# Optimization experiments

Measured on AMD Instinct MI355X. Metric: run time of the kernel, lower is better.

Reference implementation:

```python
import jax, jax.numpy as jnp
import numpy as np

N0, N1, N2 = 80000, 40000, 20000
E1, E2 = 500000, 250000
FIN = 128        # in_channels
H = 2            # heads
C1 = 64          # hidden_channels -> layer1 out per head (concat -> 128)
C2 = 64          # out_channels -> layer2 out per head (mean over heads)
ED = 10          # edge_dim per embedding, total edge feat = 2*ED = 20
NTYPE, NTS = 23, 1158


def setup_inputs() -> dict:
    key = jax.random.key(0)
    ks = jax.random.split(key, 48)
    sc = 0.05
    inp = {
        "x": jax.random.normal(ks[0], (N0, FIN), jnp.float32),
        "ei1_src": jax.random.randint(ks[1], (E1,), 0, N0),
        "ei1_dst": jax.random.randint(ks[2], (E1,), 0, N1),
        "et1": jax.random.randint(ks[3], (E1,), 0, NTYPE),
        "ets1": jax.random.randint(ks[4], (E1,), 0, NTS),
        "ei2_src": jax.random.randint(ks[5], (E2,), 0, N1),
        "ei2_dst": jax.random.randint(ks[6], (E2,), 0, N2),
        "et2": jax.random.randint(ks[7], (E2,), 0, NTYPE),
        "ets2": jax.random.randint(ks[8], (E2,), 0, NTS),
        # shared edge embeddings (Linear(23,10), Linear(1158,10))
        "edge_W": jax.random.normal(ks[9], (ED, NTYPE), jnp.float32) * sc,
        "edge_b": jax.random.normal(ks[10], (ED,), jnp.float32) * sc,
        "time_W": jax.random.normal(ks[11], (ED, NTS), jnp.float32) * sc,
        "time_b": jax.random.normal(ks[12], (ED,), jnp.float32) * sc,
    }
    # layer 1: in=128, heads=2, C=64, concat=True (out dim 128)
    hc1 = H * C1
    inp["Wq1"] = jax.random.normal(ks[13], (hc1, FIN), jnp.float32) * sc
    inp["bq1"] = jnp.zeros((hc1,), jnp.float32)
    inp["Wk1"] = jax.random.normal(ks[14], (hc1, FIN), jnp.float32) * sc
    inp["bk1"] = jnp.zeros((hc1,), jnp.float32)
    inp["Wv1"] = jax.random.normal(ks[15], (hc1, FIN), jnp.float32) * sc
    inp["bv1"] = jnp.zeros((hc1,), jnp.float32)
    inp["We1"] = jax.random.normal(ks[16], (hc1, 2 * ED), jnp.float32) * sc
    inp["Wskip1"] = jax.random.normal(ks[17], (hc1, FIN), jnp.float32) * sc
    inp["bskip1"] = jnp.zeros((hc1,), jnp.float32)
    inp["Wbeta1"] = jax.random.normal(ks[18], (1, 3 * hc1), jnp.float32) * sc
    inp["ln_g"] = jnp.ones((hc1,), jnp.float32)
    inp["ln_b"] = jnp.zeros((hc1,), jnp.float32)
    # layer 2: in=128, heads=2, C=64, concat=False (out dim 64)
    hc2 = H * C2
    inp["Wq2"] = jax.random.normal(ks[19], (hc2, hc1), jnp.float32) * sc
    inp["bq2"] = jnp.zeros((hc2,), jnp.float32)
    inp["Wk2"] = jax.random.normal(ks[20], (hc2, hc1), jnp.float32) * sc
    inp["bk2"] = jnp.zeros((hc2,), jnp.float32)
    inp["Wv2"] = jax.random.normal(ks[21], (hc2, hc1), jnp.float32) * sc
    inp["bv2"] = jnp.zeros((hc2,), jnp.float32)
    inp["We2"] = jax.random.normal(ks[22], (hc2, 2 * ED), jnp.float32) * sc
    inp["Wskip2"] = jax.random.normal(ks[23], (C2, hc1), jnp.float32) * sc
    inp["bskip2"] = jnp.zeros((C2,), jnp.float32)
    inp["Wbeta2"] = jax.random.normal(ks[24], (1, 3 * C2), jnp.float32) * sc
    return inp


def _edge_feat(et, ets, edge_W, edge_b, time_W, time_b):
    # one_hot(e) @ W.T + b == W.T[e] + b (avoids materializing huge one-hot)
    return jnp.concatenate([jnp.take(edge_W.T, et, axis=0) + edge_b,
                            jnp.take(time_W.T, ets, axis=0) + time_b], axis=-1)


def _conv(x_src, x_dst, src, dst, ef, Wq, bq, Wk, bk, Wv, bv, We,
          Wskip, bskip, Wbeta, concat):
    n_dst = x_dst.shape[0]
    HC = Wq.shape[0]
    C = HC // H
    q = (x_dst @ Wq.T + bq).reshape(n_dst, H, C)            # [Nd,H,C]
    k = (x_src @ Wk.T + bk)[src].reshape(-1, H, C)          # [E,H,C]
    v = (x_src @ Wv.T + bv)[src].reshape(-1, H, C)
    e = (ef @ We.T).reshape(-1, H, C)
    k = k + e
    alpha = jnp.einsum('ehc,ehc->eh', q[dst], k) / np.sqrt(C).astype(np.float32)
    # segment softmax over destination nodes
    m = jax.ops.segment_max(alpha, dst, num_segments=n_dst)
    ex = jnp.exp(alpha - m[dst])
    s = jax.ops.segment_sum(ex, dst, num_segments=n_dst)
    a = ex / (s[dst] + 1e-16)                               # [E,H]
    msg = (v + e) * a[..., None]                            # [E,H,C]
    out = jax.ops.segment_sum(msg.reshape(-1, HC), dst, num_segments=n_dst)
    out = out if concat else out.reshape(n_dst, H, C).mean(axis=1)
    x_r = x_dst @ Wskip.T + bskip
    beta = jax.nn.sigmoid(
        jnp.concatenate([out, x_r, out - x_r], axis=-1) @ Wbeta.T)  # [Nd,1]
    return beta * x_r + (1.0 - beta) * out


def _layernorm(x, g, b):
    mu = x.mean(-1, keepdims=True)
    var = x.var(-1, keepdims=True)
    return (x - mu) / jnp.sqrt(var + 1e-5) * g + b


def reference(x, ei1_src, ei1_dst, et1, ets1, ei2_src, ei2_dst, et2, ets2,
              edge_W, edge_b, time_W, time_b,
              Wq1, bq1, Wk1, bk1, Wv1, bv1, We1, Wskip1, bskip1, Wbeta1,
              ln_g, ln_b,
              Wq2, bq2, Wk2, bk2, Wv2, bv2, We2, Wskip2, bskip2, Wbeta2):
    ef1 = _edge_feat(et1, ets1, edge_W, edge_b, time_W, time_b)
    h = _conv(x, x[:N1], ei1_src, ei1_dst, ef1,
              Wq1, bq1, Wk1, bk1, Wv1, bv1, We1, Wskip1, bskip1, Wbeta1,
              concat=True)
    h = jax.nn.gelu(_layernorm(h, ln_g, ln_b), approximate=False)
    ef2 = _edge_feat(et2, ets2, edge_W, edge_b, time_W, time_b)
    o = _conv(h, h[:N2], ei2_src, ei2_dst, ef2,
              Wq2, bq2, Wk2, bk2, Wv2, bv2, We2, Wskip2, bskip2, Wbeta2,
              concat=False)
    return jax.nn.log_softmax(o, axis=-1)
```

## Files before the change

### kernel.cpp

```cpp
#include <hip/hip_runtime.h>
#include <math.h>

#define N0 80000
#define N1 40000
#define N2 20000
#define E1C 500000
#define E2C 250000
#define NTYPE 23
#define NTS 1158

#define NB1 157
#define NB2 79
#define KV1B 1250
#define QR1B 625
#define CNTB 2930
#define KV2B 625
#define QR2B 313
#define FILLB 2930

#define OFF_XB    0u
#define OFF_QR1   5120000u
#define OFF_KV1   15360000u
#define OFF_H     25600000u
#define OFF_QR2   28160000u
#define OFF_KV2   32000000u
#define OFF_WB1   37120000u
#define OFF_BP1   37160000u
#define OFF_WB2   37170000u
#define OFF_BP2   37200000u
#define OFF_TA1   37210000u
#define OFF_TB1   37213000u
#define OFF_TA2   37370000u
#define OFF_TB2   37373000u
#define OFF_RP1   37530000u
#define OFF_CUR1  37580000u
#define OFF_ED1   37630000u
#define OFF_BS1   38640000u
#define OFF_RP2   38650000u
#define OFF_CUR2  38680000u
#define OFF_ED2   38710000u
#define OFF_BS2   39220000u
#define OFF_DONE  39230000u
#define OFF_RK1   39240000u
#define OFF_RK2   39740000u

typedef __bf16 bf16x8 __attribute__((ext_vector_type(8)));
typedef float f32x4 __attribute__((ext_vector_type(4)));

static __device__ __forceinline__ float b2f(unsigned short u) {
    union { unsigned int i; float f; } c;
    c.i = ((unsigned int)u) << 16;
    return c.f;
}
static __device__ __forceinline__ unsigned short f2b(float f) {
    unsigned int u = __float_as_uint(f);
    unsigned int r = (u + 0x7fffu + ((u >> 16) & 1u)) >> 16;
    return (unsigned short)r;
}
static __device__ __forceinline__ bf16x8 ldfrag(const unsigned short* p) {
    return *reinterpret_cast<const bf16x8*>(p);
}

static __device__ __forceinline__ void stage16(const void* g, void* l) {
    __builtin_amdgcn_global_load_lds(
        (const __attribute__((address_space(1))) unsigned int*)g,
        (__attribute__((address_space(3))) unsigned int*)l,
        16, 0, 0);
}

template <int CTRL>
static __device__ __forceinline__ float dpp_addstep(float v) {
    int x = __builtin_amdgcn_mov_dpp(__float_as_int(v), CTRL, 0xF, 0xF, true);
    return v + __int_as_float(x);
}
static __device__ __forceinline__ float red16(float v) {
    v = dpp_addstep<0xB1>(v);
    v = dpp_addstep<0x4E>(v);
    v = dpp_addstep<0x141>(v);
    v = dpp_addstep<0x140>(v);
    return v;
}
template <int CTRL>
static __device__ __forceinline__ float dpp_maxstep(float v) {
    int x = __builtin_amdgcn_mov_dpp(__float_as_int(v), CTRL, 0xF, 0xF, true);
    return fmaxf(v, __int_as_float(x));
}
static __device__ __forceinline__ float red16max(float v) {
    v = dpp_maxstep<0xB1>(v);
    v = dpp_maxstep<0x4E>(v);
    v = dpp_maxstep<0x141>(v);
    v = dpp_maxstep<0x140>(v);
    return v;
}

#define LDSS 136
#define SMEM_USHORTS 16384

template <int NTILES>
static __device__ __forceinline__ void dev_gemm_bf16out(
    const unsigned short* __restrict__ XB, const unsigned short* __restrict__ WB,
    const float* __restrict__ BP, unsigned short* __restrict__ Y, int n, int blk,
    unsigned short* sb) {
    constexpr int COLS = NTILES * 16;
    constexpr int HALF = NTILES / 2;
    constexpr int HCOLS = HALF * 16;
    constexpr int NCHUNK = (NTILES + 7) / 8;
    int wave = threadIdx.x >> 6, lane = threadIdx.x & 63;
    int m = lane & 15, quad = lane >> 4;
    int rowbase = blk * 64 + wave * 16;
    int arow = rowbase + m; if (arow >= n) arow = n - 1;
    unsigned short* swave = sb + wave * 16 * LDSS;
    const unsigned short* xrow = XB + (size_t)arow * 128 + quad * 8;
    bf16x8 a0 = ldfrag(xrow), a1 = ldfrag(xrow + 32);
    bf16x8 a2 = ldfrag(xrow + 64), a3 = ldfrag(xrow + 96);
    f32x4 acc[NTILES];
#pragma unroll
    for (int t = 0; t < NTILES; t++) acc[t] = (f32x4){0.f, 0.f, 0.f, 0.f};
    const char* gstage = (const char*)WB + wave * 1024 + lane * 16;
    char* lstage = (char*)sb + wave * 1024;
#pragma unroll
    for (int c = 0; c < NCHUNK; c++) {
#pragma unroll
        for (int i = 0; i < 8; i++)
            if (c * 8 + i < NTILES)
                stage16(gstage + (size_t)(c * 8 + i) * 4096, lstage + i * 4096);
        __syncthreads();
#pragma unroll
        for (int t = 0; t < 8; t++) {
            if (c * 8 + t < NTILES) {
                constexpr int unused = 0; (void)unused;
                int tt = c * 8 + t;
                const unsigned short* wt = sb + t * 2048 + lane * 8;
                acc[tt] = __builtin_amdgcn_mfma_f32_16x16x32_bf16(a0, ldfrag(wt), acc[tt], 0, 0, 0);
                acc[tt] = __builtin_amdgcn_mfma_f32_16x16x32_bf16(a1, ldfrag(wt + 512), acc[tt], 0, 0, 0);
                acc[tt] = __builtin_amdgcn_mfma_f32_16x16x32_bf16(a2, ldfrag(wt + 1024), acc[tt], 0, 0, 0);
                acc[tt] = __builtin_amdgcn_mfma_f32_16x16x32_bf16(a3, ldfrag(wt + 1536), acc[tt], 0, 0, 0);
            }
        }
        __syncthreads();
    }
    int tswz_bit = (quad >> 1) & 1;
#pragma unroll
    for (int half = 0; half < 2; half++) {
#pragma unroll
        for (int t = 0; t < HALF; t++) {
            int tt = half * HALF + t;
            int tsw = t ^ tswz_bit;
            float b = BP[tt * 16 + m];
#pragma unroll
            for (int r = 0; r < 4; r++)
                swave[(quad * 4 + r) * LDSS + tsw * 16 + m] = f2b(acc[tt][r] + b);
        }
#pragma unroll
        for (int i = 0; i < 4; i++) {
            int idx = i * 64 + lane;
            int r = idx / (HCOLS / 8), g = idx % (HCOLS / 8);
            int gs = g ^ (((r >> 3) & 1) << 1);
            int grow = rowbase + r;
            if (grow < n) {
                uint4 v = *(const uint4*)&swave[r * LDSS + gs * 8];
                *(uint4*)(Y + (size_t)grow * COLS + half * HCOLS + g * 8) = v;
            }
        }
    }
}

template <int NTILES>
static __device__ __forceinline__ void dev_gemm_f32out(
    const unsigned short* __restrict__ XB, const unsigned short* __restrict__ WB,
    const float* __restrict__ BP, float* __restrict__ Y, int n, int blk,
    unsigned short* sb) {
    constexpr int COLS = NTILES * 16;
    constexpr int NCHUNK = (NTILES + 7) / 8;
    int wave = threadIdx.x >> 6, lane = threadIdx.x & 63;
    int m = lane & 15, quad = lane >> 4;
    int rowbase = blk * 64 + wave * 16;
    int arow = rowbase + m; if (arow >= n) arow = n - 1;
    const unsigned short* xrow = XB + (size_t)arow * 128 + quad * 8;
    bf16x8 a0 = ldfrag(xrow), a1 = ldfrag(xrow + 32);
    bf16x8 a2 = ldfrag(xrow + 64), a3 = ldfrag(xrow + 96);
    f32x4 acc[NTILES];
#pragma unroll
    for (int t = 0; t < NTILES; t++) acc[t] = (f32x4){0.f, 0.f, 0.f, 0.f};
    const char* gstage = (const char*)WB + wave * 1024 + lane * 16;
    char* lstage = (char*)sb + wave * 1024;
#pragma unroll
    for (int c = 0; c < NCHUNK; c++) {
#pragma unroll
        for (int i = 0; i < 8; i++)
            if (c * 8 + i < NTILES)
                stage16(gstage + (size_t)(c * 8 + i) * 4096, lstage + i * 4096);
        __syncthreads();
#pragma unroll
        for (int t = 0; t < 8; t++) {
            if (c * 8 + t < NTILES) {
                int tt = c * 8 + t;
                const unsigned short* wt = sb + t * 2048 + lane * 8;
                acc[tt] = __builtin_amdgcn_mfma_f32_16x16x32_bf16(a0, ldfrag(wt), acc[tt], 0, 0, 0);
                acc[tt] = __builtin_amdgcn_mfma_f32_16x16x32_bf16(a1, ldfrag(wt + 512), acc[tt], 0, 0, 0);
                acc[tt] = __builtin_amdgcn_mfma_f32_16x16x32_bf16(a2, ldfrag(wt + 1024), acc[tt], 0, 0, 0);
                acc[tt] = __builtin_amdgcn_mfma_f32_16x16x32_bf16(a3, ldfrag(wt + 1536), acc[tt], 0, 0, 0);
            }
        }
        __syncthreads();
    }
#pragma unroll
    for (int t = 0; t < NTILES; t++) {
        float b = BP[t * 16 + m];
#pragma unroll
        for (int r = 0; r < 4; r++) {
            int grow = rowbase + quad * 4 + r;
            if (grow < n) Y[(size_t)grow * COLS + t * 16 + m] = acc[t][r] + b;
        }
    }
}

__global__ __launch_bounds__(256) void prep(
    const float* __restrict__ x, unsigned short* __restrict__ XB,
    const float* __restrict__ Wk1, const float* __restrict__ Wv1,
    const float* __restrict__ Wq1, const float* __restrict__ Wskip1,
    const float* __restrict__ bk1, const float* __restrict__ bv1,
    const float* __restrict__ bq1, const float* __restrict__ bskip1,
    const float* __restrict__ Wk2, const float* __restrict__ Wv2,
    const float* __restrict__ Wq2, const float* __restrict__ Wskip2,
    const float* __restrict__ bk2, const float* __restrict__ bv2,
    const float* __restrict__ bq2, const float* __restrict__ bskip2,
    unsigned short* __restrict__ WB1, float* __restrict__ BP1,
    unsigned short* __restrict__ WB2, float* __restrict__ BP2,
    const float* __restrict__ edge_W, const float* __restrict__ edge_b,
    const float* __restrict__ time_W, const float* __restrict__ time_b,
    const float* __restrict__ We1, const float* __restrict__ We2,
    float* __restrict__ TA1, float* __restrict__ TB1,
    float* __restrict__ TA2, float* __restrict__ TB2,
    int* __restrict__ cnt1, int* __restrict__ cnt2, int* __restrict__ done) {
    int tid = blockIdx.x * blockDim.x + threadIdx.x;
    int stride = gridDim.x * blockDim.x;
    for (int i = tid; i < N0 * 32; i += stride) {
        float4 v = *(const float4*)(x + (size_t)i * 4);
        ushort4 u;
        u.x = f2b(v.x); u.y = f2b(v.y); u.z = f2b(v.z); u.w = f2b(v.w);
        *(ushort4*)(XB + (size_t)i * 4) = u;
    }
    for (int i = tid; i < 512 * 128; i += stride) {
        int j = i & 7, l = (i >> 3) & 63, ks = (i >> 9) & 3, t = i >> 11;
        int row = t * 16 + (l & 15);
        int col = ks * 32 + ((l >> 4) & 3) * 8 + j;
        const float* w; int off;
        if (row < 128) { w = Wk1; off = 0; }
        else if (row < 256) { w = Wv1; off = 128; }
        else if (row < 384) { w = Wq1; off = 256; }
        else { w = Wskip1; off = 384; }
        WB1[i] = f2b(w[(size_t)(row - off) * 128 + col]);
    }
    for (int i = tid; i < 512; i += stride) {
        const float* b; int off;
        if (i < 128) { b = bk1; off = 0; }
        else if (i < 256) { b = bv1; off = 128; }
        else if (i < 384) { b = bq1; off = 256; }
        else { b = bskip1; off = 384; }
        BP1[i] = b[i - off];
    }
    for (int i = tid; i < 448 * 128; i += stride) {
        int j = i & 7, l = (i >> 3) & 63, ks = (i >> 9) & 3, t = i >> 11;
        int row = t * 16 + (l & 15);
        int col = ks * 32 + ((l >> 4) & 3) * 8 + j;
        const float* w; int off;
        if (row < 128) { w = Wk2; off = 0; }
        else if (row < 256) { w = Wv2; off = 128; }
        else if (row < 384) { w = Wq2; off = 256; }
        else { w = Wskip2; off = 384; }
        WB2[i] = f2b(w[(size_t)(row - off) * 128 + col]);
    }
    for (int i = tid; i < 448; i += stride) {
        const float* b; int off;
        if (i < 128) { b = bk2; off = 0; }
        else if (i < 256) { b = bv2; off = 128; }
        else if (i < 384) { b = bq2; off = 256; }
        else { b = bskip2; off = 384; }
        BP2[i] = b[i - off];
    }
    const int TBL = (NTYPE + NTS) * 128;
    for (int i = tid; i < TBL; i += stride) {
        if (i < NTYPE * 128) {
            int e = i >> 7, c = i & 127;
            float s1 = 0.f, s2 = 0.f;
#pragma unroll
            for (int j = 0; j < 10; j++) {
                float fj = edge_W[j * NTYPE + e] + edge_b[j];
                s1 += fj * We1[c * 20 + j];
                s2 += fj * We2[c * 20 + j];
            }
            TA1[i] = s1; TA2[i] = s2;
        } else {
            int u = i - NTYPE * 128;
            int ts = u >> 7, c = u & 127;
            float s1 = 0.f, s2 = 0.f;
#pragma unroll
            for (int j = 0; j < 10; j++) {
                float fj = time_W[j * NTS + ts] + time_b[j];
                s1 += fj * We1[c * 20 + 10 + j];
                s2 += fj * We2[c * 20 + 10 + j];
            }
            TB1[u] = s1; TB2[u] = s2;
        }
    }
    for (int i = tid; i < N1 + N2 + 2; i += stride) {
        if (i < N1) cnt1[i] = 0;
        else if (i < N1 + N2) cnt2[i - N1] = 0;
        else done[i - N1 - N2] = 0;
    }
}

__global__ __launch_bounds__(256) void mega_l1(
    const unsigned short* __restrict__ XB,
    const unsigned short* __restrict__ WB1, const float* __restrict__ BP1,
    unsigned short* __restrict__ KV1, float* __restrict__ QR1,
    const int* __restrict__ d1, const int* __restrict__ d2,
    int* __restrict__ cnt1, int* __restrict__ cnt2,
    int* __restrict__ rk1, int* __restrict__ rk2) {
    __shared__ __align__(16) unsigned short sbuf[SMEM_USHORTS];
    int b = blockIdx.x;
    if (b < CNTB) {
        int t = b * 256 + threadIdx.x;
        if (t < E1C) rk1[t] = atomicAdd(&cnt1[d1[t]], 1);
        else {
            t -= E1C;
            if (t < E2C) rk2[t] = atomicAdd(&cnt2[d2[t]], 1);
        }
    } else if (b < CNTB + KV1B) {
        dev_gemm_bf16out<16>(XB, WB1, BP1, KV1, N0, b - CNTB, sbuf);
    } else {
        dev_gemm_f32out<16>(XB, WB1 + 256 * 128, BP1 + 256, QR1, N1,
                            b - CNTB - KV1B, sbuf);
    }
}

__global__ __launch_bounds__(256) void gemm_l2(
    const unsigned short* __restrict__ H,
    const unsigned short* __restrict__ WB2, const float* __restrict__ BP2,
    unsigned short* __restrict__ KV2, float* __restrict__ QR2) {
    __shared__ __align__(16) unsigned short sbuf[SMEM_USHORTS];
    int b = blockIdx.x;
    if (b < KV2B) dev_gemm_bf16out<16>(H, WB2, BP2, KV2, N1, b, sbuf);
    else dev_gemm_f32out<12>(H, WB2 + 256 * 128, BP2 + 256, QR2, N2, b - KV2B, sbuf);
}

__global__ __launch_bounds__(256) void csr_scan(
    int* __restrict__ cnt1, int* __restrict__ bs1, int* __restrict__ rp1,
    int* __restrict__ cnt2, int* __restrict__ bs2, int* __restrict__ rp2,
    int* __restrict__ done) {
    __shared__ int s[256];
    __shared__ int amlast;
    int b = blockIdx.x;
    int* cnt; int* bs; int* rp; int n, lb;
    if (b < NB1) { cnt = cnt1; bs = bs1; rp = rp1; n = N1; lb = b; }
    else { cnt = cnt2; bs = bs2; rp = rp2; n = N2; lb = b - NB1; }
    int t = lb * 256 + threadIdx.x;
    int v = (t < n) ? cnt[t] : 0;
    s[threadIdx.x] = v;
    __syncthreads();
    for (int off = 128; off; off >>= 1) {
        if (threadIdx.x < off) s[threadIdx.x] += s[threadIdx.x + off];
        __syncthreads();
    }
    if (threadIdx.x == 0) {
        atomicExch(&bs[lb], s[0]);
        __threadfence();
        int prev = atomicAdd(&done[0], 1);
        amlast = (prev == NB1 + NB2 - 1) ? 1 : 0;
    }
    __syncthreads();
    if (amlast) {
        int tt = threadIdx.x;
        int v1 = (tt < NB1) ? atomicAdd(&bs1[tt], 0) : 0;
        s[tt] = v1;
        __syncthreads();
        for (int off = 1; off < 256; off <<= 1) {
            int u = (tt >= off) ? s[tt - off] : 0;
            __syncthreads();
            s[tt] += u;
            __syncthreads();
        }
        if (tt < NB1) atomicExch(&bs1[tt], s[tt] - v1);
        __syncthreads();
        int v2 = (tt < NB2) ? atomicAdd(&bs2[tt], 0) : 0;
        s[tt] = v2;
        __syncthreads();
        for (int off = 1; off < 256; off <<= 1) {
            int u = (tt >= off) ? s[tt - off] : 0;
            __syncthreads();
            s[tt] += u;
            __syncthreads();
        }
        if (tt < NB2) atomicExch(&bs2[tt], s[tt] - v2);
        __threadfence();
        __syncthreads();
        if (tt == 0) atomicExch(&done[1], 1);
    }
    if (threadIdx.x == 0) {
        while (atomicAdd(&done[1], 0) == 0) __builtin_amdgcn_s_sleep(1);
    }
    __syncthreads();
    __threadfence();
    int base = atomicAdd(&bs[lb], 0);
    s[threadIdx.x] = v;
    __syncthreads();
    for (int off = 1; off < 256; off <<= 1) {
        int u = (threadIdx.x >= off) ? s[threadIdx.x - off] : 0;
        __syncthreads();
        s[threadIdx.x] += u;
        __syncthreads();
    }
    int incl = s[threadIdx.x];
    if (t < n) rp[t] = base + incl - v;
    if (t == n - 1) rp[n] = base + incl;
}

__global__ __launch_bounds__(256) void fill_both(
    const int* __restrict__ d1, const int* __restrict__ s1,
    const int* __restrict__ et1, const int* __restrict__ ets1,
    const int* __restrict__ rp1, const int* __restrict__ rk1, uint2* __restrict__ ed1,
    const int* __restrict__ d2, const int* __restrict__ s2,
    const int* __restrict__ et2, const int* __restrict__ ets2,
    const int* __restrict__ rp2, const int* __restrict__ rk2, uint2* __restrict__ ed2) {
    int t = blockIdx.x * 256 + threadIdx.x;
    if (t < E1C) {
        int pos = rp1[d1[t]] + rk1[t];
        ed1[pos] = make_uint2((unsigned)s1[t],
                              (unsigned)(et1[t] | (ets1[t] << 16)));
    } else {
        t -= E1C;
        if (t < E2C) {
            int pos = rp2[d2[t]] + rk2[t];
            ed2[pos] = make_uint2((unsigned)s2[t],
                                  (unsigned)(et2[t] | (ets2[t] << 16)));
        }
    }
}

__global__ __launch_bounds__(256) void agg_layer1(
    const int* __restrict__ rowptr, const uint2* __restrict__ ED,
    const float* __restrict__ TA, const float* __restrict__ TB,
    const float* __restrict__ QR, const unsigned short* __restrict__ KV,
    const float* __restrict__ Wbeta,
    const float* __restrict__ ln_g, const float* __restrict__ ln_b,
    unsigned short* __restrict__ hout, int n) {
    int wid = (blockIdx.x * blockDim.x + threadIdx.x) >> 6;
    int lane = threadIdx.x & 63;
    if (wid >= n) return;
    int s = lane >> 5, cg = lane & 15;
    int co = ((lane >> 4) & 1) * 64 + 4 * cg;
    int beg = rowptr[wid], end = rowptr[wid + 1];
    float4 q4 = *(const float4*)(QR + (size_t)wid * 256 + co);
    float ax = 0.f, ay = 0.f, az = 0.f, aw = 0.f, suma = 0.f;
    int p = beg + s;
    if (p < end) {
        uint2 d0 = ED[p];
        int pA = p + 2;  bool mA = pA < end;
        uint2 d1 = ED[mA ? pA : beg];
        int pB = p + 4;  bool mB = pB < end;
        uint2 d2 = ED[mB ? pB : beg];
        int sn0 = (int)d0.x, t0 = (int)(d0.y & 0xFFFF), ts0 = (int)(d0.y >> 16);
        float4 ta0 = *(const float4*)(TA + t0 * 128 + co);
        float4 tb0 = *(const float4*)(TB + ts0 * 128 + co);
        const unsigned short* kv0 = KV + (size_t)sn0 * 256;
        ushort4 ku0 = *(const ushort4*)(kv0 + co);
        ushort4 vu0 = *(const ushort4*)(kv0 + 128 + co);
        int sn1 = (int)d1.x, t1 = (int)(d1.y & 0xFFFF), ts1 = (int)(d1.y >> 16);
        float4 ta1 = *(const float4*)(TA + t1 * 128 + co);
        float4 tb1 = *(const float4*)(TB + ts1 * 128 + co);
        const unsigned short* kv1 = KV + (size_t)sn1 * 256;
        ushort4 ku1 = *(const ushort4*)(kv1 + co);
        ushort4 vu1 = *(const ushort4*)(kv1 + 128 + co);
        for (;;) {
            int pC = pB + 2; bool mC = pC < end;
            uint2 d3 = ED[mC ? pC : beg];
            int sn2 = (int)d2.x, t2 = (int)(d2.y & 0xFFFF), ts2 = (int)(d2.y >> 16);
            float4 ta2 = *(const float4*)(TA + t2 * 128 + co);
            float4 tb2 = *(const float4*)(TB + ts2 * 128 + co);
            const unsigned short* kv2 = KV + (size_t)sn2 * 256;
            ushort4 ku2 = *(const ushort4*)(kv2 + co);
            ushort4 vu2 = *(const ushort4*)(kv2 + 128 + co);
            float e0c = ta0.x + tb0.x, e1c = ta0.y + tb0.y;
            float e2c = ta0.z + tb0.z, e3c = ta0.w + tb0.w;
            float pp = q4.x * (b2f(ku0.x) + e0c) + q4.y * (b2f(ku0.y) + e1c)
                     + q4.z * (b2f(ku0.z) + e2c) + q4.w * (b2f(ku0.w) + e3c);
            pp = red16(pp);
            float a = __expf(pp * 0.125f);
            ax += a * (b2f(vu0.x) + e0c); ay += a * (b2f(vu0.y) + e1c);
            az += a * (b2f(vu0.z) + e2c); aw += a * (b2f(vu0.w) + e3c);
            suma += a;
            if (!mA) break;
            ta0 = ta1; tb0 = tb1; ku0 = ku1; vu0 = vu1;
            ta1 = ta2; tb1 = tb2; ku1 = ku2; vu1 = vu2;
            d2 = d3;
            mA = mB; mB = mC; pB = pC;
        }
    }
    ax += __shfl_xor(ax, 32); ay += __shfl_xor(ay, 32);
    az += __shfl_xor(az, 32); aw += __shfl_xor(aw, 32);
    suma += __shfl_xor(suma, 32);
    float inv_s = 1.f / (suma + 1e-16f);
    float ox = ax * inv_s, oy = ay * inv_s, oz = az * inv_s, ow = aw * inv_s;
    float4 r4 = *(const float4*)(QR + (size_t)wid * 256 + 128 + co);
    float4 wo = *(const float4*)(Wbeta + co);
    float4 wr = *(const float4*)(Wbeta + 128 + co);
    float4 wd = *(const float4*)(Wbeta + 256 + co);
    float pb = wo.x * ox + wr.x * r4.x + wd.x * (ox - r4.x)
             + wo.y * oy + wr.y * r4.y + wd.y * (oy - r4.y)
             + wo.z * oz + wr.z * r4.z + wd.z * (oz - r4.z)
             + wo.w * ow + wr.w * r4.w + wd.w * (ow - r4.w);
    pb = red16(pb);
    pb += __shfl_xor(pb, 16);
    float beta = 1.f / (1.f + __expf(-pb));
    float gx = beta * r4.x + (1.f - beta) * ox;
    float gy = beta * r4.y + (1.f - beta) * oy;
    float gz = beta * r4.z + (1.f - beta) * oz;
    float gw = beta * r4.w + (1.f - beta) * ow;
    float sm = gx + gy + gz + gw;
    float sq = gx * gx + gy * gy + gz * gz + gw * gw;
    sm = red16(sm); sm += __shfl_xor(sm, 16);
    sq = red16(sq); sq += __shfl_xor(sq, 16);
    float mu = sm * (1.f / 128.f);
    float var = sq * (1.f / 128.f) - mu * mu;
    float inv = rsqrtf(var + 1e-5f);
    float4 lg = *(const float4*)(ln_g + co);
    float4 lb = *(const float4*)(ln_b + co);
    float yx = (gx - mu) * inv * lg.x + lb.x;
    float yy = (gy - mu) * inv * lg.y + lb.y;
    float yz = (gz - mu) * inv * lg.z + lb.z;
    float yw = (gw - mu) * inv * lg.w + lb.w;
    const float ISQ2 = 0.70710678118654752f;
    yx = 0.5f * yx * (1.f + erff(yx * ISQ2));
    yy = 0.5f * yy * (1.f + erff(yy * ISQ2));
    yz = 0.5f * yz * (1.f + erff(yz * ISQ2));
    yw = 0.5f * yw * (1.f + erff(yw * ISQ2));
    if (s == 0) {
        ushort4 hv;
        hv.x = f2b(yx); hv.y = f2b(yy); hv.z = f2b(yz); hv.w = f2b(yw);
        *(ushort4*)(hout + (size_t)wid * 128 + co) = hv;
    }
}

__global__ __launch_bounds__(256) void agg_layer2(
    const int* __restrict__ rowptr, const uint2* __restrict__ ED,
    const float* __restrict__ TA, const float* __restrict__ TB,
    const float* __restrict__ QR, const unsigned short* __restrict__ KV,
    const float* __restrict__ Wbeta,
    float* __restrict__ o, int n) {
    int wid = (blockIdx.x * blockDim.x + threadIdx.x) >> 6;
    int lane = threadIdx.x & 63;
    if (wid >= n) return;
    int s = lane >> 5, cg = lane & 15;
    int co = ((lane >> 4) & 1) * 64 + 4 * cg;
    int beg = rowptr[wid], end = rowptr[wid + 1];
    float4 q4 = *(const float4*)(QR + (size_t)wid * 192 + co);
    float ax = 0.f, ay = 0.f, az = 0.f, aw = 0.f, suma = 0.f;
    int p = beg + s;
    if (p < end) {
        uint2 d0 = ED[p];
        int pA = p + 2;  bool mA = pA < end;
        uint2 d1 = ED[mA ? pA : beg];
        int pB = p + 4;  bool mB = pB < end;
        uint2 d2 = ED[mB ? pB : beg];
        int sn0 = (int)d0.x, t0 = (int)(d0.y & 0xFFFF), ts0 = (int)(d0.y >> 16);
        float4 ta0 = *(const float4*)(TA + t0 * 128 + co);
        float4 tb0 = *(const float4*)(TB + ts0 * 128 + co);
        const unsigned short* kv0 = KV + (size_t)sn0 * 256;
        ushort4 ku0 = *(const ushort4*)(kv0 + co);
        ushort4 vu0 = *(const ushort4*)(kv0 + 128 + co);
        int sn1 = (int)d1.x, t1 = (int)(d1.y & 0xFFFF), ts1 = (int)(d1.y >> 16);
        float4 ta1 = *(const float4*)(TA + t1 * 128 + co);
        float4 tb1 = *(const float4*)(TB + ts1 * 128 + co);
        const unsigned short* kv1 = KV + (size_t)sn1 * 256;
        ushort4 ku1 = *(const ushort4*)(kv1 + co);
        ushort4 vu1 = *(const ushort4*)(kv1 + 128 + co);
        for (;;) {
            int pC = pB + 2; bool mC = pC < end;
            uint2 d3 = ED[mC ? pC : beg];
            int sn2 = (int)d2.x, t2 = (int)(d2.y & 0xFFFF), ts2 = (int)(d2.y >> 16);
            float4 ta2 = *(const float4*)(TA + t2 * 128 + co);
            float4 tb2 = *(const float4*)(TB + ts2 * 128 + co);
            const unsigned short* kv2 = KV + (size_t)sn2 * 256;
            ushort4 ku2 = *(const ushort4*)(kv2 + co);
            ushort4 vu2 = *(const ushort4*)(kv2 + 128 + co);
            float e0c = ta0.x + tb0.x, e1c = ta0.y + tb0.y;
            float e2c = ta0.z + tb0.z, e3c = ta0.w + tb0.w;
            float pp = q4.x * (b2f(ku0.x) + e0c) + q4.y * (b2f(ku0.y) + e1c)
                     + q4.z * (b2f(ku0.z) + e2c) + q4.w * (b2f(ku0.w) + e3c);
            pp = red16(pp);
            float a = __expf(pp * 0.125f);
            ax += a * (b2f(vu0.x) + e0c); ay += a * (b2f(vu0.y) + e1c);
            az += a * (b2f(vu0.z) + e2c); aw += a * (b2f(vu0.w) + e3c);
            suma += a;
            if (!mA) break;
            ta0 = ta1; tb0 = tb1; ku0 = ku1; vu0 = vu1;
            ta1 = ta2; tb1 = tb2; ku1 = ku2; vu1 = vu2;
            d2 = d3;
            mA = mB; mB = mC; pB = pC;
        }
    }
    ax += __shfl_xor(ax, 32); ay += __shfl_xor(ay, 32);
    az += __shfl_xor(az, 32); aw += __shfl_xor(aw, 32);
    suma += __shfl_xor(suma, 32);
    float inv_s = 1.f / (suma + 1e-16f);
    float ox = ax * inv_s, oy = ay * inv_s, oz = az * inv_s, ow = aw * inv_s;
    ox = 0.5f * (ox + __shfl_xor(ox, 16));
    oy = 0.5f * (oy + __shfl_xor(oy, 16));
    oz = 0.5f * (oz + __shfl_xor(oz, 16));
    ow = 0.5f * (ow + __shfl_xor(ow, 16));
    float4 r4 = *(const float4*)(QR + (size_t)wid * 192 + 128 + 4 * cg);
    float4 wo = *(const float4*)(Wbeta + 4 * cg);
    float4 wr = *(const float4*)(Wbeta + 64 + 4 * cg);
    float4 wd = *(const float4*)(Wbeta + 128 + 4 * cg);
    float pb = wo.x * ox + wr.x * r4.x + wd.x * (ox - r4.x)
             + wo.y * oy + wr.y * r4.y + wd.y * (oy - r4.y)
             + wo.z * oz + wr.z * r4.z + wd.z * (oz - r4.z)
             + wo.w * ow + wr.w * r4.w + wd.w * (ow - r4.w);
    pb = red16(pb);
    float beta = 1.f / (1.f + __expf(-pb));
    float vx = beta * r4.x + (1.f - beta) * ox;
    float vy = beta * r4.y + (1.f - beta) * oy;
    float vz = beta * r4.z + (1.f - beta) * oz;
    float vw = beta * r4.w + (1.f - beta) * ow;
    float m = fmaxf(fmaxf(vx, vy), fmaxf(vz, vw));
    m = red16max(m);
    float se = __expf(vx - m) + __expf(vy - m) + __expf(vz - m) + __expf(vw - m);
    se = red16(se);
    float lse = m + logf(se);
    if (lane < 16)
        *(float4*)(o + (size_t)wid * 64 + 4 * cg) =
            make_float4(vx - lse, vy - lse, vz - lse, vw - lse);
}

extern "C" void kernel_launch(void* const* d_in, const int* in_sizes, int n_in,
                              void* d_out, int out_size, void* d_ws, size_t ws_size,
                              hipStream_t stream) {
    const float* x        = (const float*)d_in[0];
    const int*   ei1_src  = (const int*)d_in[1];
    const int*   ei1_dst  = (const int*)d_in[2];
    const int*   et1      = (const int*)d_in[3];
    const int*   ets1     = (const int*)d_in[4];
    const int*   ei2_src  = (const int*)d_in[5];
    const int*   ei2_dst  = (const int*)d_in[6];
    const int*   et2      = (const int*)d_in[7];
    const int*   ets2     = (const int*)d_in[8];
    const float* edge_W   = (const float*)d_in[9];
    const float* edge_b   = (const float*)d_in[10];
    const float* time_W   = (const float*)d_in[11];
    const float* time_b   = (const float*)d_in[12];
    const float* Wq1      = (const float*)d_in[13];
    const float* bq1      = (const float*)d_in[14];
    const float* Wk1      = (const float*)d_in[15];
    const float* bk1      = (const float*)d_in[16];
    const float* Wv1      = (const float*)d_in[17];
    const float* bv1      = (const float*)d_in[18];
    const float* We1      = (const float*)d_in[19];
    const float* Wskip1   = (const float*)d_in[20];
    const float* bskip1   = (const float*)d_in[21];
    const float* Wbeta1   = (const float*)d_in[22];
    const float* ln_g     = (const float*)d_in[23];
    const float* ln_b     = (const float*)d_in[24];
    const float* Wq2      = (const float*)d_in[25];
    const float* bq2      = (const float*)d_in[26];
    const float* Wk2      = (const float*)d_in[27];
    const float* bk2      = (const float*)d_in[28];
    const float* Wv2      = (const float*)d_in[29];
    const float* bv2      = (const float*)d_in[30];
    const float* We2      = (const float*)d_in[31];
    const float* Wskip2   = (const float*)d_in[32];
    const float* bskip2   = (const float*)d_in[33];
    const float* Wbeta2   = (const float*)d_in[34];

    float* ws = (float*)d_ws;
    unsigned short* xb  = (unsigned short*)(ws + OFF_XB);
    float* qr1          = ws + OFF_QR1;
    unsigned short* kv1 = (unsigned short*)(ws + OFF_KV1);
    unsigned short* h   = (unsigned short*)(ws + OFF_H);
    float* qr2          = ws + OFF_QR2;
    unsigned short* kv2 = (unsigned short*)(ws + OFF_KV2);
    unsigned short* wb1 = (unsigned short*)(ws + OFF_WB1);
    float* bp1          = ws + OFF_BP1;
    unsigned short* wb2 = (unsigned short*)(ws + OFF_WB2);
    float* bp2          = ws + OFF_BP2;
    float* ta1          = ws + OFF_TA1;
    float* tb1          = ws + OFF_TB1;
    float* ta2          = ws + OFF_TA2;
    float* tb2          = ws + OFF_TB2;
    int*   rp1          = (int*)(ws + OFF_RP1);
    int*   cur1         = (int*)(ws + OFF_CUR1);
    uint2* ed1          = (uint2*)(ws + OFF_ED1);
    int*   bs1          = (int*)(ws + OFF_BS1);
    int*   rp2          = (int*)(ws + OFF_RP2);
    int*   cur2         = (int*)(ws + OFF_CUR2);
    uint2* ed2          = (uint2*)(ws + OFF_ED2);
    int*   bs2          = (int*)(ws + OFF_BS2);
    int*   done         = (int*)(ws + OFF_DONE);
    int*   rk1          = (int*)(ws + OFF_RK1);
    int*   rk2          = (int*)(ws + OFF_RK2);

    prep<<<2048, 256, 0, stream>>>(
        x, xb,
        Wk1, Wv1, Wq1, Wskip1, bk1, bv1, bq1, bskip1,
        Wk2, Wv2, Wq2, Wskip2, bk2, bv2, bq2, bskip2,
        wb1, bp1, wb2, bp2,
        edge_W, edge_b, time_W, time_b, We1, We2,
        ta1, tb1, ta2, tb2, cur1, cur2, done);
    mega_l1<<<KV1B + QR1B + CNTB, 256, 0, stream>>>(
        xb, wb1, bp1, kv1, qr1, ei1_dst, ei2_dst, cur1, cur2, rk1, rk2);
    csr_scan<<<NB1 + NB2, 256, 0, stream>>>(cur1, bs1, rp1, cur2, bs2, rp2, done);
    fill_both<<<FILLB, 256, 0, stream>>>(
        ei1_dst, ei1_src, et1, ets1, rp1, rk1, ed1,
        ei2_dst, ei2_src, et2, ets2, rp2, rk2, ed2);
    agg_layer1<<<(N1 + 3) / 4, 256, 0, stream>>>(rp1, ed1,
        ta1, tb1, qr1, kv1, Wbeta1, ln_g, ln_b, h, N1);
    gemm_l2<<<KV2B + QR2B, 256, 0, stream>>>(h, wb2, bp2, kv2, qr2);
    agg_layer2<<<(N2 + 3) / 4, 256, 0, stream>>>(rp2, ed2,
        ta2, tb2, qr2, kv2, Wbeta2, (float*)d_out, N2);
}
```

Before: 350.3 us.

## Double-buffer GEMM weight staging, fuse CSR scan with fill, rotate edge pipeline

The GEMM helpers now stage weights in 4-tile chunks into two alternating LDS buffers, so the next chunk is prefetched while MFMAs run on the current one. The CSR scan and edge-fill kernels are merged into one kernel that waits on a grid-wide atomic barrier (a new done[2] counter) before a grid-stride fill loop, which removes one launch. The aggregation loops move into a shared helper that rotates three register sets instead of copying them each iteration. Risks: the software grid barrier deadlocks unless all 236 blocks are co-resident, and the fused fill runs on far fewer blocks than before.

```diff
diff --git a/kernel.cpp b/kernel.cpp
--- a/kernel.cpp
+++ b/kernel.cpp
@@ -16,7 +16,6 @@
 #define CNTB 2930
 #define KV2B 625
 #define QR2B 313
-#define FILLB 2930
 
 #define OFF_XB    0u
 #define OFF_QR1   5120000u
@@ -104,7 +103,7 @@
     constexpr int COLS = NTILES * 16;
     constexpr int HALF = NTILES / 2;
     constexpr int HCOLS = HALF * 16;
-    constexpr int NCHUNK = (NTILES + 7) / 8;
+    constexpr int NCHUNK = (NTILES + 3) / 4;
     int wave = threadIdx.x >> 6, lane = threadIdx.x & 63;
     int m = lane & 15, quad = lane >> 4;
     int rowbase = blk * 64 + wave * 16;
@@ -117,20 +116,26 @@
 #pragma unroll
     for (int t = 0; t < NTILES; t++) acc[t] = (f32x4){0.f, 0.f, 0.f, 0.f};
     const char* gstage = (const char*)WB + wave * 1024 + lane * 16;
-    char* lstage = (char*)sb + wave * 1024;
+#pragma unroll
+    for (int i = 0; i < 4; i++)
+        stage16(gstage + (size_t)i * 4096, (char*)sb + wave * 1024 + i * 4096);
+    __syncthreads();
 #pragma unroll
     for (int c = 0; c < NCHUNK; c++) {
-#pragma unroll
-        for (int i = 0; i < 8; i++)
-            if (c * 8 + i < NTILES)
-                stage16(gstage + (size_t)(c * 8 + i) * 4096, lstage + i * 4096);
-        __syncthreads();
-#pragma unroll
-        for (int t = 0; t < 8; t++) {
-            if (c * 8 + t < NTILES) {
-                constexpr int unused = 0; (void)unused;
-                int tt = c * 8 + t;
-                const unsigned short* wt = sb + t * 2048 + lane * 8;
+        if (c + 1 < NCHUNK) {
+            char* lbase = (char*)sb + ((c + 1) & 1) * 16384 + wave * 1024;
+#pragma unroll
+            for (int i = 0; i < 4; i++)
+                if ((c + 1) * 4 + i < NTILES)
+                    stage16(gstage + (size_t)((c + 1) * 4 + i) * 4096,
+                            lbase + i * 4096);
+        }
+        const unsigned short* cbase = sb + (c & 1) * 8192;
+#pragma unroll
+        for (int t = 0; t < 4; t++) {
+            int tt = c * 4 + t;
+            if (tt < NTILES) {
+                const unsigned short* wt = cbase + t * 2048 + lane * 8;
                 acc[tt] = __builtin_amdgcn_mfma_f32_16x16x32_bf16(a0, ldfrag(wt), acc[tt], 0, 0, 0);
                 acc[tt] = __builtin_amdgcn_mfma_f32_16x16x32_bf16(a1, ldfrag(wt + 512), acc[tt], 0, 0, 0);
                 acc[tt] = __builtin_amdgcn_mfma_f32_16x16x32_bf16(a2, ldfrag(wt + 1024), acc[tt], 0, 0, 0);
@@ -171,7 +176,7 @@
     const float* __restrict__ BP, float* __restrict__ Y, int n, int blk,
     unsigned short* sb) {
     constexpr int COLS = NTILES * 16;
-    constexpr int NCHUNK = (NTILES + 7) / 8;
+    constexpr int NCHUNK = (NTILES + 3) / 4;
     int wave = threadIdx.x >> 6, lane = threadIdx.x & 63;
     int m = lane & 15, quad = lane >> 4;
     int rowbase = blk * 64 + wave * 16;
@@ -183,19 +188,26 @@
 #pragma unroll
     for (int t = 0; t < NTILES; t++) acc[t] = (f32x4){0.f, 0.f, 0.f, 0.f};
     const char* gstage = (const char*)WB + wave * 1024 + lane * 16;
-    char* lstage = (char*)sb + wave * 1024;
+#pragma unroll
+    for (int i = 0; i < 4; i++)
+        stage16(gstage + (size_t)i * 4096, (char*)sb + wave * 1024 + i * 4096);
+    __syncthreads();
 #pragma unroll
     for (int c = 0; c < NCHUNK; c++) {
-#pragma unroll
-        for (int i = 0; i < 8; i++)
-            if (c * 8 + i < NTILES)
-                stage16(gstage + (size_t)(c * 8 + i) * 4096, lstage + i * 4096);
-        __syncthreads();
-#pragma unroll
-        for (int t = 0; t < 8; t++) {
-            if (c * 8 + t < NTILES) {
-                int tt = c * 8 + t;
-                const unsigned short* wt = sb + t * 2048 + lane * 8;
+        if (c + 1 < NCHUNK) {
+            char* lbase = (char*)sb + ((c + 1) & 1) * 16384 + wave * 1024;
+#pragma unroll
+            for (int i = 0; i < 4; i++)
+                if ((c + 1) * 4 + i < NTILES)
+                    stage16(gstage + (size_t)((c + 1) * 4 + i) * 4096,
+                            lbase + i * 4096);
+        }
+        const unsigned short* cbase = sb + (c & 1) * 8192;
+#pragma unroll
+        for (int t = 0; t < 4; t++) {
+            int tt = c * 4 + t;
+            if (tt < NTILES) {
+                const unsigned short* wt = cbase + t * 2048 + lane * 8;
                 acc[tt] = __builtin_amdgcn_mfma_f32_16x16x32_bf16(a0, ldfrag(wt), acc[tt], 0, 0, 0);
                 acc[tt] = __builtin_amdgcn_mfma_f32_16x16x32_bf16(a1, ldfrag(wt + 512), acc[tt], 0, 0, 0);
                 acc[tt] = __builtin_amdgcn_mfma_f32_16x16x32_bf16(a2, ldfrag(wt + 1024), acc[tt], 0, 0, 0);
@@ -304,7 +316,7 @@
             TB1[u] = s1; TB2[u] = s2;
         }
     }
-    for (int i = tid; i < N1 + N2 + 2; i += stride) {
+    for (int i = tid; i < N1 + N2 + 3; i += stride) {
         if (i < N1) cnt1[i] = 0;
         else if (i < N1 + N2) cnt2[i - N1] = 0;
         else done[i - N1 - N2] = 0;
@@ -345,10 +357,16 @@
     else dev_gemm_f32out<12>(H, WB2 + 256 * 128, BP2 + 256, QR2, N2, b - KV2B, sbuf);
 }
 
-__global__ __launch_bounds__(256) void csr_scan(
+__global__ __launch_bounds__(256) void csr_scan_fill(
     int* __restrict__ cnt1, int* __restrict__ bs1, int* __restrict__ rp1,
     int* __restrict__ cnt2, int* __restrict__ bs2, int* __restrict__ rp2,
-    int* __restrict__ done) {
+    int* __restrict__ done,
+    const int* __restrict__ d1, const int* __restrict__ s1,
+    const int* __restrict__ et1, const int* __restrict__ ets1,
+    const int* __restrict__ rk1, uint2* __restrict__ ed1,
+    const int* __restrict__ d2, const int* __restrict__ s2,
+    const int* __restrict__ et2, const int* __restrict__ ets2,
+    const int* __restrict__ rk2, uint2* __restrict__ ed2) {
     __shared__ int s[256];
     __shared__ int amlast;
     int b = blockIdx.x;
@@ -414,28 +432,97 @@
     int incl = s[threadIdx.x];
     if (t < n) rp[t] = base + incl - v;
     if (t == n - 1) rp[n] = base + incl;
-}
-
-__global__ __launch_bounds__(256) void fill_both(
-    const int* __restrict__ d1, const int* __restrict__ s1,
-    const int* __restrict__ et1, const int* __restrict__ ets1,
-    const int* __restrict__ rp1, const int* __restrict__ rk1, uint2* __restrict__ ed1,
-    const int* __restrict__ d2, const int* __restrict__ s2,
-    const int* __restrict__ et2, const int* __restrict__ ets2,
-    const int* __restrict__ rp2, const int* __restrict__ rk2, uint2* __restrict__ ed2) {
-    int t = blockIdx.x * 256 + threadIdx.x;
-    if (t < E1C) {
-        int pos = rp1[d1[t]] + rk1[t];
-        ed1[pos] = make_uint2((unsigned)s1[t],
-                              (unsigned)(et1[t] | (ets1[t] << 16)));
-    } else {
-        t -= E1C;
-        if (t < E2C) {
-            int pos = rp2[d2[t]] + rk2[t];
-            ed2[pos] = make_uint2((unsigned)s2[t],
-                                  (unsigned)(et2[t] | (ets2[t] << 16)));
-        }
-    }
+    __threadfence();
+    __syncthreads();
+    if (threadIdx.x == 0) {
+        atomicAdd(&done[2], 1);
+        while (atomicAdd(&done[2], 0) < NB1 + NB2) __builtin_amdgcn_s_sleep(1);
+    }
+    __syncthreads();
+    __threadfence();
+    const int total = E1C + E2C;
+    const int gstride = (NB1 + NB2) * 256;
+    for (int te = blockIdx.x * 256 + threadIdx.x; te < total; te += gstride) {
+        if (te < E1C) {
+            int pos = rp1[d1[te]] + rk1[te];
+            ed1[pos] = make_uint2((unsigned)s1[te],
+                                  (unsigned)(et1[te] | (ets1[te] << 16)));
+        } else {
+            int u = te - E1C;
+            int pos = rp2[d2[u]] + rk2[u];
+            ed2[pos] = make_uint2((unsigned)s2[u],
+                                  (unsigned)(et2[u] | (ets2[u] << 16)));
+        }
+    }
+}
+
+static __device__ __forceinline__ void edge_accum(
+    int beg, int end, int s, int co, float4 q4,
+    const uint2* __restrict__ ED, const float* __restrict__ TA,
+    const float* __restrict__ TB, const unsigned short* __restrict__ KV,
+    float& ax, float& ay, float& az, float& aw, float& suma) {
+    int p = beg + s;
+    if (p >= end) return;
+
+    uint2 dA, dB, dC;
+    float4 taA, tbA, taB, tbB, taC, tbC;
+    ushort4 kuA, vuA, kuB, vuB, kuC, vuC;
+
+    dA = ED[p];
+    int pA = p + 2; bool mA = pA < end;
+    dB = ED[mA ? pA : beg];
+    int pB = p + 4; bool mB = pB < end;
+    dC = ED[mB ? pB : beg];
+
+#define LOADSET(SET, DSC) { \
+    int sn_ = (int)DSC.x, t_ = (int)(DSC.y & 0xFFFF), ts_ = (int)(DSC.y >> 16); \
+    ta##SET = *(const float4*)(TA + t_ * 128 + co); \
+    tb##SET = *(const float4*)(TB + ts_ * 128 + co); \
+    const unsigned short* kv_ = KV + (size_t)sn_ * 256; \
+    ku##SET = *(const ushort4*)(kv_ + co); \
+    vu##SET = *(const ushort4*)(kv_ + 128 + co); }
+
+#define COMPUTE(SET) { \
+    float e0c = ta##SET.x + tb##SET.x, e1c = ta##SET.y + tb##SET.y; \
+    float e2c = ta##SET.z + tb##SET.z, e3c = ta##SET.w + tb##SET.w; \
+    float pp = q4.x * (b2f(ku##SET.x) + e0c) + q4.y * (b2f(ku##SET.y) + e1c) \
+             + q4.z * (b2f(ku##SET.z) + e2c) + q4.w * (b2f(ku##SET.w) + e3c); \
+    pp = red16(pp); \
+    float a = __expf(pp * 0.125f); \
+    ax += a * (b2f(vu##SET.x) + e0c); ay += a * (b2f(vu##SET.y) + e1c); \
+    az += a * (b2f(vu##SET.z) + e2c); aw += a * (b2f(vu##SET.w) + e3c); \
+    suma += a; }
+
+    LOADSET(A, dA)
+    LOADSET(B, dB)
+    for (;;) {
+        {
+            int pC = pB + 2; bool mC = pC < end;
+            dA = ED[mC ? pC : beg];
+            LOADSET(C, dC)
+            COMPUTE(A)
+            if (!mA) break;
+            mA = mB; mB = mC; pB = pC;
+        }
+        {
+            int pC = pB + 2; bool mC = pC < end;
+            dB = ED[mC ? pC : beg];
+            LOADSET(A, dA)
+            COMPUTE(B)
+            if (!mA) break;
+            mA = mB; mB = mC; pB = pC;
+        }
+        {
+            int pC = pB + 2; bool mC = pC < end;
+            dC = ED[mC ? pC : beg];
+            LOADSET(B, dB)
+            COMPUTE(C)
+            if (!mA) break;
+            mA = mB; mB = mC; pB = pC;
+        }
+    }
+#undef LOADSET
+#undef COMPUTE
 }
 
 __global__ __launch_bounds__(256) void agg_layer1(
@@ -453,50 +540,7 @@
     int beg = rowptr[wid], end = rowptr[wid + 1];
     float4 q4 = *(const float4*)(QR + (size_t)wid * 256 + co);
     float ax = 0.f, ay = 0.f, az = 0.f, aw = 0.f, suma = 0.f;
-    int p = beg + s;
-    if (p < end) {
-        uint2 d0 = ED[p];
-        int pA = p + 2;  bool mA = pA < end;
-        uint2 d1 = ED[mA ? pA : beg];
-        int pB = p + 4;  bool mB = pB < end;
-        uint2 d2 = ED[mB ? pB : beg];
-        int sn0 = (int)d0.x, t0 = (int)(d0.y & 0xFFFF), ts0 = (int)(d0.y >> 16);
-        float4 ta0 = *(const float4*)(TA + t0 * 128 + co);
-        float4 tb0 = *(const float4*)(TB + ts0 * 128 + co);
-        const unsigned short* kv0 = KV + (size_t)sn0 * 256;
-        ushort4 ku0 = *(const ushort4*)(kv0 + co);
-        ushort4 vu0 = *(const ushort4*)(kv0 + 128 + co);
-        int sn1 = (int)d1.x, t1 = (int)(d1.y & 0xFFFF), ts1 = (int)(d1.y >> 16);
-        float4 ta1 = *(const float4*)(TA + t1 * 128 + co);
-        float4 tb1 = *(const float4*)(TB + ts1 * 128 + co);
-        const unsigned short* kv1 = KV + (size_t)sn1 * 256;
-        ushort4 ku1 = *(const ushort4*)(kv1 + co);
-        ushort4 vu1 = *(const ushort4*)(kv1 + 128 + co);
-        for (;;) {
-            int pC = pB + 2; bool mC = pC < end;
-            uint2 d3 = ED[mC ? pC : beg];
-            int sn2 = (int)d2.x, t2 = (int)(d2.y & 0xFFFF), ts2 = (int)(d2.y >> 16);
-            float4 ta2 = *(const float4*)(TA + t2 * 128 + co);
-            float4 tb2 = *(const float4*)(TB + ts2 * 128 + co);
-            const unsigned short* kv2 = KV + (size_t)sn2 * 256;
-            ushort4 ku2 = *(const ushort4*)(kv2 + co);
-            ushort4 vu2 = *(const ushort4*)(kv2 + 128 + co);
-            float e0c = ta0.x + tb0.x, e1c = ta0.y + tb0.y;
-            float e2c = ta0.z + tb0.z, e3c = ta0.w + tb0.w;
-            float pp = q4.x * (b2f(ku0.x) + e0c) + q4.y * (b2f(ku0.y) + e1c)
-                     + q4.z * (b2f(ku0.z) + e2c) + q4.w * (b2f(ku0.w) + e3c);
-            pp = red16(pp);
-            float a = __expf(pp * 0.125f);
-            ax += a * (b2f(vu0.x) + e0c); ay += a * (b2f(vu0.y) + e1c);
-            az += a * (b2f(vu0.z) + e2c); aw += a * (b2f(vu0.w) + e3c);
-            suma += a;
-            if (!mA) break;
-            ta0 = ta1; tb0 = tb1; ku0 = ku1; vu0 = vu1;
-            ta1 = ta2; tb1 = tb2; ku1 = ku2; vu1 = vu2;
-            d2 = d3;
-            mA = mB; mB = mC; pB = pC;
-        }
-    }
+    edge_accum(beg, end, s, co, q4, ED, TA, TB, KV, ax, ay, az, aw, suma);
     ax += __shfl_xor(ax, 32); ay += __shfl_xor(ay, 32);
     az += __shfl_xor(az, 32); aw += __shfl_xor(aw, 32);
     suma += __shfl_xor(suma, 32);
@@ -556,50 +600,7 @@
     int beg = rowptr[wid], end = rowptr[wid + 1];
     float4 q4 = *(const float4*)(QR + (size_t)wid * 192 + co);
     float ax = 0.f, ay = 0.f, az = 0.f, aw = 0.f, suma = 0.f;
-    int p = beg + s;
-    if (p < end) {
-        uint2 d0 = ED[p];
-        int pA = p + 2;  bool mA = pA < end;
-        uint2 d1 = ED[mA ? pA : beg];
-        int pB = p + 4;  bool mB = pB < end;
-        uint2 d2 = ED[mB ? pB : beg];
-        int sn0 = (int)d0.x, t0 = (int)(d0.y & 0xFFFF), ts0 = (int)(d0.y >> 16);
-        float4 ta0 = *(const float4*)(TA + t0 * 128 + co);
-        float4 tb0 = *(const float4*)(TB + ts0 * 128 + co);
-        const unsigned short* kv0 = KV + (size_t)sn0 * 256;
-        ushort4 ku0 = *(const ushort4*)(kv0 + co);
-        ushort4 vu0 = *(const ushort4*)(kv0 + 128 + co);
-        int sn1 = (int)d1.x, t1 = (int)(d1.y & 0xFFFF), ts1 = (int)(d1.y >> 16);
-        float4 ta1 = *(const float4*)(TA + t1 * 128 + co);
-        float4 tb1 = *(const float4*)(TB + ts1 * 128 + co);
-        const unsigned short* kv1 = KV + (size_t)sn1 * 256;
-        ushort4 ku1 = *(const ushort4*)(kv1 + co);
-        ushort4 vu1 = *(const ushort4*)(kv1 + 128 + co);
-        for (;;) {
-            int pC = pB + 2; bool mC = pC < end;
-            uint2 d3 = ED[mC ? pC : beg];
-            int sn2 = (int)d2.x, t2 = (int)(d2.y & 0xFFFF), ts2 = (int)(d2.y >> 16);
-            float4 ta2 = *(const float4*)(TA + t2 * 128 + co);
-            float4 tb2 = *(const float4*)(TB + ts2 * 128 + co);
-            const unsigned short* kv2 = KV + (size_t)sn2 * 256;
-            ushort4 ku2 = *(const ushort4*)(kv2 + co);
-            ushort4 vu2 = *(const ushort4*)(kv2 + 128 + co);
-            float e0c = ta0.x + tb0.x, e1c = ta0.y + tb0.y;
-            float e2c = ta0.z + tb0.z, e3c = ta0.w + tb0.w;
-            float pp = q4.x * (b2f(ku0.x) + e0c) + q4.y * (b2f(ku0.y) + e1c)
-                     + q4.z * (b2f(ku0.z) + e2c) + q4.w * (b2f(ku0.w) + e3c);
-            pp = red16(pp);
-            float a = __expf(pp * 0.125f);
-            ax += a * (b2f(vu0.x) + e0c); ay += a * (b2f(vu0.y) + e1c);
-            az += a * (b2f(vu0.z) + e2c); aw += a * (b2f(vu0.w) + e3c);
-            suma += a;
-            if (!mA) break;
-            ta0 = ta1; tb0 = tb1; ku0 = ku1; vu0 = vu1;
-            ta1 = ta2; tb1 = tb2; ku1 = ku2; vu1 = vu2;
-            d2 = d3;
-            mA = mB; mB = mC; pB = pC;
-        }
-    }
+    edge_accum(beg, end, s, co, q4, ED, TA, TB, KV, ax, ay, az, aw, suma);
     ax += __shfl_xor(ax, 32); ay += __shfl_xor(ay, 32);
     az += __shfl_xor(az, 32); aw += __shfl_xor(aw, 32);
     suma += __shfl_xor(suma, 32);
@@ -708,10 +709,10 @@
         ta1, tb1, ta2, tb2, cur1, cur2, done);
     mega_l1<<<KV1B + QR1B + CNTB, 256, 0, stream>>>(
         xb, wb1, bp1, kv1, qr1, ei1_dst, ei2_dst, cur1, cur2, rk1, rk2);
-    csr_scan<<<NB1 + NB2, 256, 0, stream>>>(cur1, bs1, rp1, cur2, bs2, rp2, done);
-    fill_both<<<FILLB, 256, 0, stream>>>(
-        ei1_dst, ei1_src, et1, ets1, rp1, rk1, ed1,
-        ei2_dst, ei2_src, et2, ets2, rp2, rk2, ed2);
+    csr_scan_fill<<<NB1 + NB2, 256, 0, stream>>>(
+        cur1, bs1, rp1, cur2, bs2, rp2, done,
+        ei1_dst, ei1_src, et1, ets1, rk1, ed1,
+        ei2_dst, ei2_src, et2, ets2, rk2, ed2);
     agg_layer1<<<(N1 + 3) / 4, 256, 0, stream>>>(rp1, ed1,
         ta1, tb1, qr1, kv1, Wbeta1, ln_g, ln_b, h, N1);
     gemm_l2<<<KV2B + QR2B, 256, 0, stream>>>(h, wb2, bp2, kv2, qr2);
```

New measurement: 398.3 us. +13.7%, slower.
